# Optimization experiments

Measured on AMD Instinct MI355X. Metric: run time of the kernel, lower is better.

## Reference

```python
import jax, jax.numpy as jnp
import numpy as np

B, N = 32, 512
TOKEN_DIM, FEAT_DIM = 256, 3133


def setup_inputs() -> dict:
    key = jax.random.key(0)
    ks = jax.random.split(key, 7)
    embeddings = jax.random.normal(ks[0], (B, N, 3072), dtype=jnp.float32)
    visibility_scores = jax.random.uniform(ks[1], (B, N, 6), dtype=jnp.float32)
    bbox_ltwh = jax.random.uniform(ks[2], (B, N, 4), dtype=jnp.float32)
    keypoints_xyc = jax.random.uniform(ks[3], (B, N, 17, 3), dtype=jnp.float32)
    feats_masks = jax.random.randint(ks[4], (B, N), 0, 2).astype(jnp.bool_)
    # nn.Linear(feat_dim, token_dim): W [out,in], b [out]
    bound = 1.0 / np.sqrt(FEAT_DIM)
    W = jax.random.uniform(ks[5], (TOKEN_DIM, FEAT_DIM), minval=-bound, maxval=bound, dtype=jnp.float32)
    b = jax.random.uniform(ks[6], (TOKEN_DIM,), minval=-bound, maxval=bound, dtype=jnp.float32)
    return {
        'embeddings': embeddings,
        'visibility_scores': visibility_scores,
        'bbox_ltwh': bbox_ltwh,
        'keypoints_xyc': keypoints_xyc,
        'feats_masks': feats_masks,
        'W': W,
        'b': b,
    }


def reference(embeddings, visibility_scores, bbox_ltwh, keypoints_xyc, feats_masks, W, b):
    Bm, Nm = feats_masks.shape
    kpts_flat = keypoints_xyc.reshape(Bm, Nm, -1)  # [B,N,51]
    cat_feats = jnp.concatenate([embeddings, visibility_scores, bbox_ltwh, kpts_flat], axis=-1)  # [B,N,3133]
    # gather -> linear -> scatter into zeros  ==  masked linear output
    y = jnp.einsum('bnf,tf->bnt', cat_feats, W) + b  # [B,N,token_dim]
    tokens = jnp.where(feats_masks[..., None], y, jnp.zeros((), dtype=y.dtype))
    return tokens
```

## Files before the change

### kernel.cpp

```cpp
#include <hip/hip_runtime.h>
#include <hip/hip_bf16.h>


#define TOKENS   16384
#define EMB      3072
#define KF       3133
#define TDIM     256
#define NSTEP    49
#define BM       64
#define BT       128
#define WIMG     16384

typedef __attribute__((ext_vector_type(8))) short bf16x8;
typedef __attribute__((ext_vector_type(4))) float f32x4;

__device__ __forceinline__ unsigned int f2bf(float f) {
  __hip_bfloat16 h = __float2bfloat16(f);
  unsigned short u;
  __builtin_memcpy(&u, &h, 2);
  return (unsigned int)u;
}
__device__ __forceinline__ unsigned int pack2(float a, float b) {
  return f2bf(a) | (f2bf(b) << 16);
}
__device__ __forceinline__ bf16x8 cvt8(float4 a, float4 b) {
  union { unsigned int u[4]; bf16x8 v; } r;
  r.u[0] = pack2(a.x, a.y);
  r.u[1] = pack2(a.z, a.w);
  r.u[2] = pack2(b.x, b.y);
  r.u[3] = pack2(b.z, b.w);
  return r.v;
}

__device__ __forceinline__ void g2l16(const void* g, void* l) {
  __builtin_amdgcn_global_load_lds(
      (__attribute__((address_space(1))) void*)g,
      (__attribute__((address_space(3))) void*)l,
      16, 0, 0);
}

__global__ void pack_w_kernel(const float* __restrict__ W, unsigned short* __restrict__ wq) {
  int i = blockIdx.x * 256 + threadIdx.x;
  if (i >= 2 * NSTEP * 8192) return;
  int tt  = i / (NSTEP * 8192);
  int r   = i % (NSTEP * 8192);
  int s   = r >> 13;
  int e   = r & 8191;
  int row = e >> 6;
  int cs  = e & 63;
  int c   = cs ^ ((row & 7) << 3);
  int k   = s * 64 + c;
  int t   = tt * BT + row;
  float v = (k < KF) ? W[(size_t)t * KF + k] : 0.f;
  __hip_bfloat16 h = __float2bfloat16(v);
  unsigned short u; __builtin_memcpy(&u, &h, 2);
  wq[i] = u;
}

__global__ void pack_ext_kernel(const float* __restrict__ vis,
                                const float* __restrict__ bbox,
                                const float* __restrict__ kpt,
                                float* __restrict__ ext) {
  int i = blockIdx.x * 256 + threadIdx.x;
  int bn = i >> 6;
  int j  = i & 63;
  float v = 0.f;
  if (j < 6)       v = vis[bn * 6 + j];
  else if (j < 10) v = bbox[bn * 4 + (j - 6)];
  else if (j < 61) v = kpt[bn * 51 + (j - 10)];
  ext[i] = v;
}

__global__ __launch_bounds__(256, 2)
void linproj_kernel(const float* __restrict__ emb,
                    const int* __restrict__ mask,
                    const unsigned short* __restrict__ wqp,
                    const float* __restrict__ ext,
                    const float* __restrict__ bias,
                    float* __restrict__ out) {
  __shared__ unsigned short ldsW[2 * 8192];

  const int tid = threadIdx.x;
  const int bid = blockIdx.x;
  const int mtile = ((bid >> 4) << 3) | (bid & 7);
  const int ttile = (bid >> 3) & 1;
  const int mBase = mtile * BM;
  const int tBase = ttile * BT;

  const int lane = tid & 63;
  const int wid  = tid >> 6;
  const int wm   = (wid >> 1) * 32;
  const int wt   = (wid & 1) * 64;
  const int lr   = lane & 15;
  const int lk   = lane >> 4;

  const int row0 = mBase + wm + lr;
  const int row1 = row0 + 16;
  const bool m0 = (mask[row0] != 0);
  const bool m1 = (mask[row1] != 0);
  const int aoff = lk * 8;
  const float* pA0 = emb + (size_t)row0 * EMB + aoff;
  const float* pA1 = emb + (size_t)row1 * EMB + aoff;
  const float* pE0 = ext + (size_t)row0 * 64 + aoff;
  const float* pE1 = ext + (size_t)row1 * 64 + aoff;

  const char* wsrc = (const char*)wqp + (size_t)ttile * (NSTEP * WIMG)
                   + wid * 1024 + lane * 16;
  char* lbase = (char*)ldsW;

  const int swz0 = (lk * 16) ^ ((lr & 7) << 4);
  const int swz1 = (64 + lk * 16) ^ ((lr & 7) << 4);
  const int rbase = (wt + lr) * 128;

  f32x4 acc[2][4];
#pragma unroll
  for (int m = 0; m < 2; ++m)
#pragma unroll
    for (int t = 0; t < 4; ++t)
      acc[m][t] = (f32x4){0.f, 0.f, 0.f, 0.f};

  float4 Aa[2][2][2], Ab[2][2][2];

  auto stageW = [&](int s, int buf) {
    const char* g = wsrc + (size_t)s * WIMG;
    char* l = lbase + buf * WIMG + wid * 1024;
#pragma unroll
    for (int j = 0; j < 4; ++j)
      g2l16(g + j * 4096, l + j * 4096);
  };

  auto loadA = [&](int s, float4 (&A)[2][2][2]) {
    const float* p0;
    const float* p1;
    if (s < NSTEP - 1) { p0 = pA0 + s * 64; p1 = pA1 + s * 64; }
    else               { p0 = pE0;          p1 = pE1; }
    if (m0) {
#pragma unroll
      for (int kk = 0; kk < 2; ++kk) {
        A[0][kk][0] = *(const float4*)(p0 + kk * 32);
        A[0][kk][1] = *(const float4*)(p0 + kk * 32 + 4);
      }
    } else {
#pragma unroll
      for (int kk = 0; kk < 2; ++kk)
        A[0][kk][0] = A[0][kk][1] = make_float4(0.f, 0.f, 0.f, 0.f);
    }
    if (m1) {
#pragma unroll
      for (int kk = 0; kk < 2; ++kk) {
        A[1][kk][0] = *(const float4*)(p1 + kk * 32);
        A[1][kk][1] = *(const float4*)(p1 + kk * 32 + 4);
      }
    } else {
#pragma unroll
      for (int kk = 0; kk < 2; ++kk)
        A[1][kk][0] = A[1][kk][1] = make_float4(0.f, 0.f, 0.f, 0.f);
    }
  };

  auto compute = [&](int buf, const float4 (&A)[2][2][2]) {
    const char* l = lbase + buf * WIMG;
#pragma unroll
    for (int kk = 0; kk < 2; ++kk) {
      bf16x8 a0 = cvt8(A[0][kk][0], A[0][kk][1]);
      bf16x8 a1 = cvt8(A[1][kk][0], A[1][kk][1]);
      const int sw = kk ? swz1 : swz0;
#pragma unroll
      for (int tf = 0; tf < 4; ++tf) {
        bf16x8 bv = *(const bf16x8*)(l + rbase + tf * 2048 + sw);
        acc[0][tf] = __builtin_amdgcn_mfma_f32_16x16x32_bf16(a0, bv, acc[0][tf], 0, 0, 0);
        acc[1][tf] = __builtin_amdgcn_mfma_f32_16x16x32_bf16(a1, bv, acc[1][tf], 0, 0, 0);
      }
    }
  };

  stageW(0, 0);
  loadA(0, Aa);
  __syncthreads();

#pragma unroll 1
  for (int s = 0; s < NSTEP - 1; s += 2) {
    stageW(s + 1, 1);
    loadA(s + 1, Ab);
    compute(0, Aa);
    __syncthreads();
    stageW(s + 2, 0);
    loadA(s + 2, Aa);
    compute(1, Ab);
    __syncthreads();
  }
  compute(0, Aa);

#pragma unroll
  for (int tf = 0; tf < 4; ++tf) {
    const int t = tBase + wt + tf * 16 + lr;
    const float bv = bias[t];
#pragma unroll
    for (int mf = 0; mf < 2; ++mf) {
#pragma unroll
      for (int r = 0; r < 4; ++r) {
        const int bn = mBase + wm + mf * 16 + lk * 4 + r;
        out[(size_t)bn * TDIM + t] = (mask[bn] != 0) ? (acc[mf][tf][r] + bv) : 0.f;
      }
    }
  }
}

extern "C" void kernel_launch(void* const* d_in, const int* in_sizes, int n_in,
                              void* d_out, int out_size, void* d_ws, size_t ws_size,
                              hipStream_t stream) {
  const float* emb   = (const float*)d_in[0];
  const float* vis   = (const float*)d_in[1];
  const float* bbox  = (const float*)d_in[2];
  const float* kpt   = (const float*)d_in[3];
  const int*   mask  = (const int*)d_in[4];
  const float* W     = (const float*)d_in[5];
  const float* bias  = (const float*)d_in[6];
  float* out = (float*)d_out;

  float* ext          = (float*)d_ws;
  unsigned short* wq  = (unsigned short*)((char*)d_ws + (size_t)TOKENS * 64 * 4);

  pack_w_kernel  <<<(2 * NSTEP * 8192 + 255) / 256, 256, 0, stream>>>(W, wq);
  pack_ext_kernel<<<(TOKENS * 64) / 256,            256, 0, stream>>>(vis, bbox, kpt, ext);
  linproj_kernel <<<512, 256, 0, stream>>>(emb, mask, wq, ext, bias, out);
}
```

Before: 321.8 us.

## Double-step LDS pipeline with four weight buffers and branchless masked A loads

Grows LDS staging from two to four weight buffers and processes two K-steps per barrier, with register prefetch of A for two steps at a time. This halves the number of __syncthreads and deepens prefetch to hide global-load latency. The K-step count is padded to an even number (one zero-weight step), and masked rows now read real data from a redirected address instead of branching to zeros. The result is still zeroed at the store, but this adds memory traffic for masked rows and doubles LDS use per block, which may limit occupancy.

```diff
diff --git a/kernel.cpp b/kernel.cpp
--- a/kernel.cpp
+++ b/kernel.cpp
@@ -6,7 +6,7 @@
 #define EMB      3072
 #define KF       3133
 #define TDIM     256
-#define NSTEP    49
+#define NS       50
 #define BM       64
 #define BT       128
 #define WIMG     16384
@@ -41,9 +41,9 @@
 
 __global__ void pack_w_kernel(const float* __restrict__ W, unsigned short* __restrict__ wq) {
   int i = blockIdx.x * 256 + threadIdx.x;
-  if (i >= 2 * NSTEP * 8192) return;
-  int tt  = i / (NSTEP * 8192);
-  int r   = i % (NSTEP * 8192);
+  if (i >= 2 * NS * 8192) return;
+  int tt  = i / (NS * 8192);
+  int r   = i % (NS * 8192);
   int s   = r >> 13;
   int e   = r & 8191;
   int row = e >> 6;
@@ -78,7 +78,7 @@
                     const float* __restrict__ ext,
                     const float* __restrict__ bias,
                     float* __restrict__ out) {
-  __shared__ unsigned short ldsW[2 * 8192];
+  __shared__ unsigned short ldsW[4 * 8192];
 
   const int tid = threadIdx.x;
   const int bid = blockIdx.x;
@@ -99,12 +99,12 @@
   const bool m0 = (mask[row0] != 0);
   const bool m1 = (mask[row1] != 0);
   const int aoff = lk * 8;
-  const float* pA0 = emb + (size_t)row0 * EMB + aoff;
-  const float* pA1 = emb + (size_t)row1 * EMB + aoff;
-  const float* pE0 = ext + (size_t)row0 * 64 + aoff;
-  const float* pE1 = ext + (size_t)row1 * 64 + aoff;
-
-  const char* wsrc = (const char*)wqp + (size_t)ttile * (NSTEP * WIMG)
+  const float* pA0 = (m0 ? emb + (size_t)row0 * EMB : emb) + aoff;
+  const float* pA1 = (m1 ? emb + (size_t)row1 * EMB : emb) + aoff;
+  const float* pE0 = (m0 ? ext + (size_t)row0 * 64 : ext) + aoff;
+  const float* pE1 = (m1 ? ext + (size_t)row1 * 64 : ext) + aoff;
+
+  const char* wsrc = (const char*)wqp + (size_t)ttile * (NS * WIMG)
                    + wid * 1024 + lane * 16;
   char* lbase = (char*)ldsW;
 
@@ -119,7 +119,7 @@
     for (int t = 0; t < 4; ++t)
       acc[m][t] = (f32x4){0.f, 0.f, 0.f, 0.f};
 
-  float4 Aa[2][2][2], Ab[2][2][2];
+  float4 Aa[2][2][2][2], Ab[2][2][2][2];
 
   auto stageW = [&](int s, int buf) {
     const char* g = wsrc + (size_t)s * WIMG;
@@ -128,38 +128,28 @@
     for (int j = 0; j < 4; ++j)
       g2l16(g + j * 4096, l + j * 4096);
   };
-
-  auto loadA = [&](int s, float4 (&A)[2][2][2]) {
-    const float* p0;
-    const float* p1;
-    if (s < NSTEP - 1) { p0 = pA0 + s * 64; p1 = pA1 + s * 64; }
-    else               { p0 = pE0;          p1 = pE1; }
-    if (m0) {
+  auto stage2 = [&](int s0, int bp) {
+    if (s0 < NS) { stageW(s0, bp * 2); stageW(s0 + 1, bp * 2 + 1); }
+  };
+
+  auto loadA2 = [&](int s0, float4 (&A)[2][2][2][2]) {
+#pragma unroll
+    for (int st = 0; st < 2; ++st) {
+      const int s = s0 + st;
+      const float* q0 = (s < NS - 2) ? (pA0 + s * 64) : pE0;
+      const float* q1 = (s < NS - 2) ? (pA1 + s * 64) : pE1;
 #pragma unroll
       for (int kk = 0; kk < 2; ++kk) {
-        A[0][kk][0] = *(const float4*)(p0 + kk * 32);
-        A[0][kk][1] = *(const float4*)(p0 + kk * 32 + 4);
+        A[st][0][kk][0] = *(const float4*)(q0 + kk * 32);
+        A[st][0][kk][1] = *(const float4*)(q0 + kk * 32 + 4);
+        A[st][1][kk][0] = *(const float4*)(q1 + kk * 32);
+        A[st][1][kk][1] = *(const float4*)(q1 + kk * 32 + 4);
       }
-    } else {
-#pragma unroll
-      for (int kk = 0; kk < 2; ++kk)
-        A[0][kk][0] = A[0][kk][1] = make_float4(0.f, 0.f, 0.f, 0.f);
     }
-    if (m1) {
-#pragma unroll
-      for (int kk = 0; kk < 2; ++kk) {
-        A[1][kk][0] = *(const float4*)(p1 + kk * 32);
-        A[1][kk][1] = *(const float4*)(p1 + kk * 32 + 4);
-      }
-    } else {
-#pragma unroll
-      for (int kk = 0; kk < 2; ++kk)
-        A[1][kk][0] = A[1][kk][1] = make_float4(0.f, 0.f, 0.f, 0.f);
-    }
-  };
-
-  auto compute = [&](int buf, const float4 (&A)[2][2][2]) {
-    const char* l = lbase + buf * WIMG;
+  };
+
+  auto computeStep = [&](int b, const float4 (&A)[2][2][2]) {
+    const char* l = lbase + b * WIMG;
 #pragma unroll
     for (int kk = 0; kk < 2; ++kk) {
       bf16x8 a0 = cvt8(A[0][kk][0], A[0][kk][1]);
@@ -174,22 +164,26 @@
     }
   };
 
-  stageW(0, 0);
-  loadA(0, Aa);
+  stage2(0, 0);
+  stage2(2, 1);
+  loadA2(0, Aa);
   __syncthreads();
 
 #pragma unroll 1
-  for (int s = 0; s < NSTEP - 1; s += 2) {
-    stageW(s + 1, 1);
-    loadA(s + 1, Ab);
-    compute(0, Aa);
+  for (int g = 0; g < 24; g += 2) {
+    loadA2(2 * g + 2, Ab);
+    computeStep(0, Aa[0]);
+    computeStep(1, Aa[1]);
     __syncthreads();
-    stageW(s + 2, 0);
-    loadA(s + 2, Aa);
-    compute(1, Ab);
+    stage2(2 * g + 4, 0);
+    loadA2(2 * g + 4, Aa);
+    computeStep(2, Ab[0]);
+    computeStep(3, Ab[1]);
     __syncthreads();
+    stage2(2 * g + 6, 1);
   }
-  compute(0, Aa);
+  computeStep(0, Aa[0]);
+  computeStep(1, Aa[1]);
 
 #pragma unroll
   for (int tf = 0; tf < 4; ++tf) {
@@ -221,7 +215,7 @@
   float* ext          = (float*)d_ws;
   unsigned short* wq  = (unsigned short*)((char*)d_ws + (size_t)TOKENS * 64 * 4);
 
-  pack_w_kernel  <<<(2 * NSTEP * 8192 + 255) / 256, 256, 0, stream>>>(W, wq);
-  pack_ext_kernel<<<(TOKENS * 64) / 256,            256, 0, stream>>>(vis, bbox, kpt, ext);
+  pack_w_kernel  <<<(2 * NS * 8192 + 255) / 256, 256, 0, stream>>>(W, wq);
+  pack_ext_kernel<<<(TOKENS * 64) / 256,         256, 0, stream>>>(vis, bbox, kpt, ext);
   linproj_kernel <<<512, 256, 0, stream>>>(emb, mask, wq, ext, bias, out);
 }
```

After: 346.2 us. 7.6% more time.
